# Kernel optimization log

Hardware: AMD Instinct MI355X
Metric: run time of the kernel (lower is better)

Reference implementation:

```python
import jax, jax.numpy as jnp
import numpy as np

# dims: batch, cdd_size, his_size, signal_length, embedding_dim, filter_num, top-k, levels, vocab
B, CDD, HIS, S, E, F, K, L, VOCAB = 32, 5, 50, 20, 300, 150, 30, 3, 50000


def _conv1d(x, w, b, d):
    # x: [N, C_in, S], w: [C_out, C_in, 3], 'same' length via padding=d, dilation=d
    y = jax.lax.conv_general_dilated(x, w, (1,), [(d, d)], rhs_dilation=(d,),
                                     dimension_numbers=('NCW', 'OIW', 'NCW'))
    return y + b[None, :, None]


def _conv3d(x, w, b):
    # x: [N, C_in, D, H, W], padding 1 on all spatial dims
    y = jax.lax.conv_general_dilated(x, w, (1, 1, 1), [(1, 1)] * 3,
                                     dimension_numbers=('NCDHW', 'OIDHW', 'NCDHW'))
    return y + b[None, :, None, None, None]


def _maxpool3(x):
    return jax.lax.reduce_window(x, -jnp.inf, jax.lax.max,
                                 (1, 1, 3, 3, 3), (1, 1, 3, 3, 3), 'VALID')


def setup_inputs() -> dict:
    key = jax.random.key(0)
    ks = jax.random.split(key, 12)
    n = lambda k, s, sc=0.05: jax.random.normal(k, s, dtype=jnp.float32) * sc
    return {
        'candidate_title': jax.random.randint(ks[0], (B, CDD, S), 0, VOCAB),
        'clicked_title': jax.random.randint(ks[1], (B, HIS, S), 0, VOCAB),
        'his_mask': jnp.zeros((B, HIS, 1), dtype=bool),
        'embedding': n(ks[2], (VOCAB, E), 0.1),
        'w1': n(ks[3], (F, E, 3)), 'b1': jnp.zeros((F,), jnp.float32),
        'w2': n(ks[4], (F, F, 3)), 'b2': jnp.zeros((F,), jnp.float32),
        'w3': n(ks[5], (F, F, 3)), 'b3': jnp.zeros((F,), jnp.float32),
        'ln_w': jnp.ones((F,), jnp.float32), 'ln_b': jnp.zeros((F,), jnp.float32),
        'q_words': n(ks[6], (1, F), 1.0), 'q_levels': n(ks[7], (1, F), 1.0),
        'c3d_w1': n(ks[8], (32, L, 3, 3, 3)), 'c3d_b1': jnp.zeros((32,), jnp.float32),
        'c3d_w2': n(ks[9], (16, 32, 3, 3, 3)), 'c3d_b2': jnp.zeros((16,), jnp.float32),
        'ltr_w': n(ks[10], (1, 192)), 'ltr_b': jnp.zeros((1,), jnp.float32),
    }


def reference(candidate_title, clicked_title, his_mask, embedding,
              w1, b1, w2, b2, w3, b3, ln_w, ln_b, q_words, q_levels,
              c3d_w1, c3d_b1, c3d_w2, c3d_b2, ltr_w, ltr_b):
    def ln(x):
        m = x.mean(-1, keepdims=True)
        v = x.var(-1, keepdims=True)  # biased var, matches torch LayerNorm
        return (x - m) / jnp.sqrt(v + 1e-5) * ln_w + ln_b

    scale_e = jnp.sqrt(jnp.float32(E))  # NOTE: original divides by sqrt(embedding_dim)

    def encode(ids):
        nn = ids.shape[1]
        x = embedding[ids].reshape(-1, S, E).transpose(0, 2, 1)  # [N, E, S] (dropout = identity at eval)
        d1 = ln(_conv1d(x, w1, b1, 1).transpose(0, 2, 1))                     # [N, S, F]
        d2 = ln(_conv1d(d1.transpose(0, 2, 1), w2, b2, 2).transpose(0, 2, 1))
        d3 = ln(_conv1d(d2.transpose(0, 2, 1), w3, b3, 3).transpose(0, 2, 1))
        dil = jnp.stack([jax.nn.relu(d1), jax.nn.relu(d2), jax.nn.relu(d3)], axis=2)  # [N, S, L, F]
        dil = dil.reshape(B, nn, S, L, F)
        # level attention with query_levels
        lw = jax.nn.softmax(jnp.einsum('bnslf,f->bnsl', dil, q_levels[0]) / scale_e, axis=-1)
        wf = jnp.einsum('bnsl,bnslf->bnsf', lw, dil)
        # word attention with query_words
        ww = jax.nn.softmax(jnp.einsum('bnsf,f->bns', wf, q_words[0]) / scale_e, axis=-1)
        reprs = jnp.einsum('bns,bnsf->bnf', ww, wf)
        return dil, reprs

    cdd_emb, cdd_repr = encode(candidate_title)   # [B,CDD,S,L,F], [B,CDD,F]
    his_emb, his_repr = encode(clicked_title)     # [B,HIS,S,L,F], [B,HIS,F]

    # news-level attention -> top-k one-hot gating (gather of history news)
    scores = jnp.einsum('bcf,bhf->bch', cdd_repr, his_repr)
    scores = jnp.where(his_mask.transpose(0, 2, 1), -jnp.inf, scores)
    attn = jax.nn.softmax(scores, axis=-1)
    _, idx = jax.lax.top_k(attn, K)                                  # [B,CDD,K]
    his_act = his_emb[jnp.arange(B)[:, None, None], idx]             # [B,CDD,K,S,L,F]

    # fusion tensor: per-level word-word interaction maps
    cdd_t = cdd_emb.transpose(0, 1, 3, 2, 4)       # [B,CDD,L,S,F]
    his_t = his_act.transpose(0, 1, 2, 4, 3, 5)    # [B,CDD,K,L,S,F]
    fusion = jnp.einsum('bclsf,bckltf->bcklst', cdd_t, his_t) / jnp.sqrt(jnp.float32(F))
    fusion = fusion.reshape(B * CDD, K, L, S, S).transpose(0, 2, 1, 3, 4)  # [B*CDD, L, K, S, S]

    h = _maxpool3(jax.nn.relu(_conv3d(fusion, c3d_w1, c3d_b1)))
    h = _maxpool3(jax.nn.relu(_conv3d(h, c3d_w2, c3d_b2)))
    feat = h.reshape(B, CDD, -1)                   # [B, CDD, 192]
    score = jnp.einsum('bcd,d->bc', feat, ltr_w[0]) + ltr_b[0]
    return jax.nn.log_softmax(score, axis=-1)
```

## Files before the change

kernel.cpp:

```cpp
#include <hip/hip_runtime.h>
#include <hip/hip_bf16.h>

#define NB   32
#define NCDD 5
#define NHIS 50
#define SS   20
#define EE   300
#define FF   150
#define KK   30
#define LL   3
#define NSEQ (NB*NCDD + NB*NHIS)
#define NCD  (NB*NCDD)
#define NROW (NSEQ*SS)
#define CONVGRID (NROW/64)

typedef unsigned short u16;
typedef __attribute__((ext_vector_type(8))) short bf16x8;
typedef __attribute__((ext_vector_type(4))) float f32x4;

__device__ __forceinline__ float b2f(u16 v) {
    union { unsigned int u; float f; } c; c.u = ((unsigned int)v) << 16; return c.f;
}
__device__ __forceinline__ u16 f2b(float f) {
    union { float f; unsigned int u; } c; c.f = f;
    unsigned int r = c.u + 0x7FFF + ((c.u >> 16) & 1);
    return (u16)(r >> 16);
}
__device__ __forceinline__ float ldf(const void* p, size_t i, int isbf) {
    return isbf ? b2f(((const u16*)p)[i]) : ((const float*)p)[i];
}
__device__ __forceinline__ float dget(const float* d, size_t i) {
    unsigned int u = ((const unsigned int*)d)[i];
    return b2f((u16)(u & 0xffffu)) + b2f((u16)(u >> 16));
}

__global__ void detect_dtype(const u16* lnw_raw, int* flag) {
    if (threadIdx.x == 0)
        flag[0] = (lnw_raw[0] == 0x3F80 && lnw_raw[1] == 0x3F80) ? 1 : 0;
}

struct CJob { const void* src; float* dst; int n; };
struct CJobs { CJob j[13]; };

__global__ __launch_bounds__(256) void convert_many(CJobs jobs, const int* flagp) {
    int isbf = flagp[0];
    CJob job = jobs.j[blockIdx.x];
    for (int i = threadIdx.x; i < job.n; i += 256) job.dst[i] = ldf(job.src, i, isbf);
}

__global__ __launch_bounds__(256) void repack_wb(const void* w, const int* flagp,
                                                 u16* outh, u16* outl,
                                                 int CIN, int KP, int CV) {
    int isbf = flagp[0];
    int i = blockIdx.x*256 + threadIdx.x;
    if (i >= 160*3*KP) return;
    int g = i % KP; int r = i / KP; int tap = r % 3; int f = r / 3;
    float v = 0.f;
    if (f < FF && g < CV) v = ldf(w, ((size_t)f*CIN + g)*3 + tap, isbf);
    u16 hi = f2b(v);
    u16 lo = f2b(v - b2f(hi));
    size_t o = (size_t)f*(3*KP) + (size_t)tap*KP + g;
    outh[o] = hi; outl[o] = lo;
}

template<int STAGE>
__global__ __launch_bounds__(256, 2) void conv_mfma(const int* __restrict__ flagp,
        const int* __restrict__ cand, const int* __restrict__ clik,
        const void* __restrict__ emb,
        const unsigned int* __restrict__ dprev,
        const u16* __restrict__ wh, const u16* __restrict__ wl,
        const float* __restrict__ bias,
        const float* __restrict__ lnw, const float* __restrict__ lnb,
        unsigned int* __restrict__ dout)
{
    constexpr int KC  = 32;
    constexpr int PAD = 40;
    constexpr int KT  = (STAGE == 0) ? 960 : 480;
    constexpr int NC  = KT / KC;
    constexpr int DIL = (STAGE == 1) ? 2 : 3;
    constexpr int ASZ = 64*PAD, BSZ = 160*PAD;
    constexpr int STG = (2*ASZ + 2*BSZ)*2;
    constexpr int SMB = (STG > 64*164*4) ? STG : 64*164*4;
    __shared__ __align__(16) char smem[SMB];
    u16* Ah = (u16*)smem;
    u16* Al = Ah + ASZ;
    u16* Bh = Al + ASZ;
    u16* Bl = Bh + BSZ;

    const int tid  = threadIdx.x;
    const int row0 = blockIdx.x * 64;
    const int lane = tid & 63, wid = tid >> 6;
    const int wm = wid >> 1, wn = wid & 1;
    const int lr = lane & 15, lk = lane >> 4;
    const int isbf = flagp[0];

    const int arow = tid >> 2, aseg = tid & 3;
    const int grow = row0 + arow;
    const int an   = grow / 20;
    const int as   = grow - an*20;
    int aid[3];
    if constexpr (STAGE == 0) {
        #pragma unroll
        for (int t = 0; t < 3; ++t) {
            int w = as + t - 1;
            aid[t] = ((unsigned)w < 20u) ? ((an < NCD) ? cand[an*SS + w] : clik[(an - NCD)*SS + w])
                                         : -1;
        }
    }

    float xa[8];
    uint4 ra32[2];
    uint4 rb[5];

    auto LOADG = [&](int c) {
        if constexpr (STAGE == 0) {
            int tap = c / 10;
            int e0  = (c - tap*10)*32 + aseg*8;
            int id  = aid[tap];
            float4 x0 = {0.f,0.f,0.f,0.f}, x1 = {0.f,0.f,0.f,0.f};
            if (id >= 0) {
                if (!isbf) {
                    const float* ep = (const float*)emb + (size_t)id*EE + e0;
                    if (e0 < EE)     x0 = *(const float4*)ep;
                    if (e0 + 4 < EE) x1 = *(const float4*)(ep + 4);
                } else {
                    const u16* ep = (const u16*)emb + (size_t)id*EE + e0;
                    float t[8];
                    #pragma unroll
                    for (int j = 0; j < 8; ++j) t[j] = (e0 + j < EE) ? b2f(ep[j]) : 0.f;
                    x0.x=t[0]; x0.y=t[1]; x0.z=t[2]; x0.w=t[3];
                    x1.x=t[4]; x1.y=t[5]; x1.z=t[6]; x1.w=t[7];
                }
            }
            xa[0]=x0.x; xa[1]=x0.y; xa[2]=x0.z; xa[3]=x0.w;
            xa[4]=x1.x; xa[5]=x1.y; xa[6]=x1.z; xa[7]=x1.w;
        } else {
            int tap = c / 5;
            int f0  = (c - tap*5)*32;
            int word = as + DIL*(tap - 1);
            int gbase = f0 + aseg*8;
            ra32[0].x=ra32[0].y=ra32[0].z=ra32[0].w=0u;
            ra32[1].x=ra32[1].y=ra32[1].z=ra32[1].w=0u;
            if ((unsigned)word < 20u && gbase < FF) {
                const unsigned int* p = dprev + (size_t)(an*SS + word)*FF + gbase;
                uint2 q0 = *(const uint2*)(p);
                uint2 q1 = *(const uint2*)(p + 2);
                uint2 q2 = *(const uint2*)(p + 4);
                uint2 q3 = *(const uint2*)(p + 6);
                ra32[0].x = q0.x; ra32[0].y = q0.y; ra32[0].z = q1.x; ra32[0].w = q1.y;
                ra32[1].x = q2.x; ra32[1].y = q2.y; ra32[1].z = q3.x; ra32[1].w = q3.y;
                if (gbase + 7 >= FF) {
                    if (gbase + 1 >= FF) ra32[0].y = 0u;
                    if (gbase + 2 >= FF) ra32[0].z = 0u;
                    if (gbase + 3 >= FF) ra32[0].w = 0u;
                    if (gbase + 4 >= FF) ra32[1].x = 0u;
                    if (gbase + 5 >= FF) ra32[1].y = 0u;
                    if (gbase + 6 >= FF) ra32[1].z = 0u;
                    ra32[1].w = 0u;
                }
            }
        }
        #pragma unroll
        for (int j = 0; j < 5; ++j) {
            int item = tid + j*256;
            const u16* wp = (item < 640) ? wh : wl;
            int rem  = (item < 640) ? item : item - 640;
            rb[j] = *(const uint4*)(wp + (size_t)(rem >> 2)*KT + c*KC + (rem & 3)*8);
        }
    };

    auto WRITE = [&]() {
        uint4 h, l;
        if constexpr (STAGE == 0) {
            u16 hh[8], lo[8];
            #pragma unroll
            for (int j = 0; j < 8; ++j) {
                hh[j] = f2b(xa[j]);
                lo[j] = f2b(xa[j] - b2f(hh[j]));
            }
            h.x = hh[0] | ((unsigned)hh[1] << 16); h.y = hh[2] | ((unsigned)hh[3] << 16);
            h.z = hh[4] | ((unsigned)hh[5] << 16); h.w = hh[6] | ((unsigned)hh[7] << 16);
            l.x = lo[0] | ((unsigned)lo[1] << 16); l.y = lo[2] | ((unsigned)lo[3] << 16);
            l.z = lo[4] | ((unsigned)lo[5] << 16); l.w = lo[6] | ((unsigned)lo[7] << 16);
        } else {
            h.x = (ra32[0].x & 0xffffu) | (ra32[0].y << 16);
            h.y = (ra32[0].z & 0xffffu) | (ra32[0].w << 16);
            h.z = (ra32[1].x & 0xffffu) | (ra32[1].y << 16);
            h.w = (ra32[1].z & 0xffffu) | (ra32[1].w << 16);
            l.x = (ra32[0].x >> 16) | (ra32[0].y & 0xffff0000u);
            l.y = (ra32[0].z >> 16) | (ra32[0].w & 0xffff0000u);
            l.z = (ra32[1].x >> 16) | (ra32[1].y & 0xffff0000u);
            l.w = (ra32[1].z >> 16) | (ra32[1].w & 0xffff0000u);
        }
        *(uint4*)(Ah + arow*PAD + aseg*8) = h;
        *(uint4*)(Al + arow*PAD + aseg*8) = l;
        #pragma unroll
        for (int j = 0; j < 5; ++j) {
            int item = tid + j*256;
            u16* bp = (item < 640) ? Bh : Bl;
            int rem = (item < 640) ? item : item - 640;
            *(uint4*)(bp + (rem >> 2)*PAD + (rem & 3)*8) = rb[j];
        }
    };

    f32x4 acc[2][5];
    #pragma unroll
    for (int mf = 0; mf < 2; ++mf)
        #pragma unroll
        for (int nf = 0; nf < 5; ++nf)
            acc[mf][nf] = (f32x4){0.f,0.f,0.f,0.f};

    auto COMPUTE = [&]() {
        bf16x8 fah[2], fal[2], fbh[5], fbl[5];
        #pragma unroll
        for (int mf = 0; mf < 2; ++mf) {
            fah[mf] = *(const bf16x8*)(Ah + (wm*32 + mf*16 + lr)*PAD + lk*8);
            fal[mf] = *(const bf16x8*)(Al + (wm*32 + mf*16 + lr)*PAD + lk*8);
        }
        #pragma unroll
        for (int nf = 0; nf < 5; ++nf) {
            fbh[nf] = *(const bf16x8*)(Bh + (wn*80 + nf*16 + lr)*PAD + lk*8);
            fbl[nf] = *(const bf16x8*)(Bl + (wn*80 + nf*16 + lr)*PAD + lk*8);
        }
        #pragma unroll
        for (int mf = 0; mf < 2; ++mf)
            #pragma unroll
            for (int nf = 0; nf < 5; ++nf)
                acc[mf][nf] = __builtin_amdgcn_mfma_f32_16x16x32_bf16(fah[mf], fbh[nf], acc[mf][nf], 0, 0, 0);
        #pragma unroll
        for (int mf = 0; mf < 2; ++mf)
            #pragma unroll
            for (int nf = 0; nf < 5; ++nf)
                acc[mf][nf] = __builtin_amdgcn_mfma_f32_16x16x32_bf16(fah[mf], fbl[nf], acc[mf][nf], 0, 0, 0);
        #pragma unroll
        for (int mf = 0; mf < 2; ++mf)
            #pragma unroll
            for (int nf = 0; nf < 5; ++nf)
                acc[mf][nf] = __builtin_amdgcn_mfma_f32_16x16x32_bf16(fal[mf], fbh[nf], acc[mf][nf], 0, 0, 0);
    };

    LOADG(0); WRITE();
    for (int c = 0; c < NC; ++c) {
        if (c + 1 < NC) LOADG(c + 1);
        __syncthreads();
        COMPUTE();
        __syncthreads();
        if (c + 1 < NC) WRITE();
    }

    float* outb = (float*)smem;
    #pragma unroll
    for (int mf = 0; mf < 2; ++mf)
        #pragma unroll
        for (int nf = 0; nf < 5; ++nf)
            #pragma unroll
            for (int r = 0; r < 4; ++r)
                outb[(wm*32 + mf*16 + lk*4 + r)*164 + wn*80 + nf*16 + lr] = acc[mf][nf][r];
    __syncthreads();

    for (int rl = wid*16; rl < wid*16 + 16; ++rl) {
        float vv[3]; float sum = 0.f, sq = 0.f;
        #pragma unroll
        for (int j = 0; j < 3; ++j) {
            int f = lane + j*64;
            float v = 0.f;
            if (f < FF) v = outb[rl*164 + f] + bias[f];
            vv[j] = v; sum += v; sq += v*v;
        }
        #pragma unroll
        for (int off = 32; off; off >>= 1) { sum += __shfl_down(sum, off); sq += __shfl_down(sq, off); }
        sum = __shfl(sum, 0); sq = __shfl(sq, 0);
        float m = sum / FF, var = sq / FF - m*m, inv = rsqrtf(var + 1e-5f);
        #pragma unroll
        for (int j = 0; j < 3; ++j) {
            int f = lane + j*64;
            if (f < FF) {
                float v = (vv[j] - m) * inv * lnw[f] + lnb[f];
                u16 hi = f2b(v);
                unsigned int lo = (unsigned int)f2b(v - b2f(hi));
                dout[(size_t)(row0 + rl)*FF + f] = (unsigned int)hi | (lo << 16);
            }
        }
    }
}

__global__ __launch_bounds__(256) void lvwd_attn(const float* d1, const float* d2, const float* d3,
                                                 const float* ql, const float* qw, float* reprs) {
    __shared__ float wfs[SS*FF];
    __shared__ float scs[SS];
    int n = blockIdx.x, tid = threadIdx.x;
    int wave = tid >> 6, lane = tid & 63;
    for (int s = wave; s < SS; s += 4) {
        size_t base = ((size_t)n*SS + s) * FF;
        float v[3][3];
        float dt[3] = {0.f, 0.f, 0.f};
        #pragma unroll
        for (int j = 0; j < 3; ++j) {
            int f = lane + j*64;
            float q = (f < FF) ? ql[f] : 0.f;
            float x0 = (f < FF) ? fmaxf(dget(d1, base+f), 0.f) : 0.f;
            float x1 = (f < FF) ? fmaxf(dget(d2, base+f), 0.f) : 0.f;
            float x2 = (f < FF) ? fmaxf(dget(d3, base+f), 0.f) : 0.f;
            v[0][j] = x0; v[1][j] = x1; v[2][j] = x2;
            dt[0] += x0*q; dt[1] += x1*q; dt[2] += x2*q;
        }
        #pragma unroll
        for (int off = 32; off; off >>= 1) {
            dt[0] += __shfl_xor(dt[0], off);
            dt[1] += __shfl_xor(dt[1], off);
            dt[2] += __shfl_xor(dt[2], off);
        }
        const float sc = 0.057735026918962584f;
        float a0 = dt[0]*sc, a1 = dt[1]*sc, a2 = dt[2]*sc;
        float mx = fmaxf(a0, fmaxf(a1, a2));
        float e0 = expf(a0-mx), e1 = expf(a1-mx), e2 = expf(a2-mx);
        float den = e0+e1+e2;
        float l0 = e0/den, l1 = e1/den, l2 = e2/den;
        #pragma unroll
        for (int j = 0; j < 3; ++j) {
            int f = lane + j*64;
            if (f < FF) wfs[s*FF + f] = l0*v[0][j] + l1*v[1][j] + l2*v[2][j];
        }
    }
    __syncthreads();
    if (wave == 0) {
        if (lane < SS) {
            float a = 0.f;
            for (int f = 0; f < FF; ++f) a += wfs[lane*FF + f]*qw[f];
            scs[lane] = a * 0.057735026918962584f;
        }
        float mx = -1e30f;
        #pragma unroll
        for (int s = 0; s < SS; ++s) mx = fmaxf(mx, scs[s]);
        float ww[SS]; float den = 0.f;
        #pragma unroll
        for (int s = 0; s < SS; ++s) { ww[s] = expf(scs[s]-mx); den += ww[s]; }
        float inv = 1.f/den;
        for (int f = lane; f < FF; f += 64) {
            float a = 0.f;
            #pragma unroll
            for (int s = 0; s < SS; ++s) a += ww[s]*wfs[s*FF + f];
            reprs[(size_t)n*FF + f] = a*inv;
        }
    }
}

__global__ __launch_bounds__(256) void score_kernel(const float* reprs, const unsigned char* mask,
                                                    float* scores) {
    int i = blockIdx.x*256 + threadIdx.x;
    if (i >= NB*NCDD*NHIS) return;
    int b = i/(NCDD*NHIS); int r = i%(NCDD*NHIS); int h = r%NHIS; int c = r/NHIS;
    const float* cr = reprs + (size_t)(b*NCDD + c)*FF;
    const float* hr = reprs + (size_t)(NCD + b*NHIS + h)*FF;
    float a = 0.f;
    for (int f = 0; f < FF; ++f) a += cr[f]*hr[f];
    if (mask[b*NHIS + h]) a = -1e30f;
    scores[i] = a;
}

__global__ __launch_bounds__(64) void topk_kernel(const float* scores, int* idx) {
    int i = blockIdx.x*64 + threadIdx.x;
    if (i >= NB*NCDD) return;
    float sc[NHIS];
    const float* sp = scores + i*NHIS;
    for (int h = 0; h < NHIS; ++h) sc[h] = sp[h];
    for (int k = 0; k < KK; ++k) {
        int best = 0; float bv = -1e38f;
        for (int h = 0; h < NHIS; ++h) { if (sc[h] > bv) { bv = sc[h]; best = h; } }
        idx[i*KK + k] = best;
        sc[best] = -1e38f;
    }
}

__global__ __launch_bounds__(256) void fusion_kernel(const float* d1, const float* d2, const float* d3,
                                                     const int* idx, float* fus) {
    constexpr int RS  = 168;
    constexpr int TSZ = 32*RS;
    __shared__ __align__(16) u16 smem[4*TSZ];
    u16* Ah = smem;
    u16* Al = smem + TSZ;
    u16* Hh = smem + 2*TSZ;
    u16* Hl = smem + 3*TSZ;
    int blk = blockIdx.x;
    int k = blk % KK; int r2 = blk / KK; int l = r2 % LL; int bc = r2 / LL;
    int b = bc / NCDD;
    int nh = NCD + b*NHIS + idx[bc*KK + k];
    const float* dl = (l == 0) ? d1 : ((l == 1) ? d2 : d3);
    const unsigned int* Ap = (const unsigned int*)dl + (size_t)bc*SS*FF;
    const unsigned int* Hp = (const unsigned int*)dl + (size_t)nh*SS*FF;
    int tid = threadIdx.x;
    for (int i = tid; i < 4*TSZ/8; i += 256)
        *(uint4*)(smem + (size_t)i*8) = (uint4){0u,0u,0u,0u};
    __syncthreads();
    for (int item = tid; item < 760; item += 256) {
        int side = item >= 380;
        int rem  = side ? item - 380 : item;
        int row  = rem / 19, f0 = (rem - row*19)*8;
        const unsigned int* p = (side ? Hp : Ap) + row*FF + f0;
        unsigned int q[8];
        #pragma unroll
        for (int j = 0; j < 8; j += 2) {
            uint2 t2 = {0u, 0u};
            if (f0 + j < FF) t2 = *(const uint2*)(p + j);
            q[j] = t2.x; q[j+1] = t2.y;
        }
        unsigned int hh[8], ll[8];
        #pragma unroll
        for (int j = 0; j < 8; ++j) {
            unsigned int u = q[j];
            float f = b2f((u16)(u & 0xffffu)) + b2f((u16)(u >> 16));
            int keep = (f > 0.f);
            hh[j] = keep ? (u & 0xffffu) : 0u;
            ll[j] = keep ? (u >> 16)     : 0u;
        }
        uint4 h, lo;
        h.x  = hh[0] | (hh[1] << 16); h.y  = hh[2] | (hh[3] << 16);
        h.z  = hh[4] | (hh[5] << 16); h.w  = hh[6] | (hh[7] << 16);
        lo.x = ll[0] | (ll[1] << 16); lo.y = ll[2] | (ll[3] << 16);
        lo.z = ll[4] | (ll[5] << 16); lo.w = ll[6] | (ll[7] << 16);
        u16* dh = (side ? Hh : Ah) + row*RS + f0;
        u16* dL = (side ? Hl : Al) + row*RS + f0;
        *(uint4*)dh = h;
        *(uint4*)dL = lo;
    }
    __syncthreads();
    const int lane = tid & 63, wid = tid >> 6;
    const int wm = wid >> 1, wn = wid & 1;
    const int lr = lane & 15, lk = lane >> 4;
    f32x4 acc = {0.f, 0.f, 0.f, 0.f};
    #pragma unroll
    for (int c = 0; c < 5; ++c) {
        bf16x8 fah = *(const bf16x8*)(Ah + (wm*16 + lr)*RS + c*32 + lk*8);
        bf16x8 fal = *(const bf16x8*)(Al + (wm*16 + lr)*RS + c*32 + lk*8);
        bf16x8 fbh = *(const bf16x8*)(Hh + (wn*16 + lr)*RS + c*32 + lk*8);
        bf16x8 fbl = *(const bf16x8*)(Hl + (wn*16 + lr)*RS + c*32 + lk*8);
        acc = __builtin_amdgcn_mfma_f32_16x16x32_bf16(fah, fbh, acc, 0, 0, 0);
        acc = __builtin_amdgcn_mfma_f32_16x16x32_bf16(fah, fbl, acc, 0, 0, 0);
        acc = __builtin_amdgcn_mfma_f32_16x16x32_bf16(fal, fbh, acc, 0, 0, 0);
    }
    #pragma unroll
    for (int r = 0; r < 4; ++r) {
        int s = wm*16 + lk*4 + r, t = wn*16 + lr;
        if (s < SS && t < SS)
            fus[(size_t)blk*400 + s*20 + t] = acc[r] * 0.08164965809277261f;
    }
}

__global__ __launch_bounds__(256) void c3d1_kernel(const float* __restrict__ fus,
                                                   const float* __restrict__ w,
                                                   const float* __restrict__ bias,
                                                   float* __restrict__ h1) {
    __shared__ float Sin[3*5*22*22];
    __shared__ float Wls[32*81];
    int blk = blockIdx.x;
    int dz = blk % 10; int bc = blk / 10;
    int tid = threadIdx.x;
    for (int i = tid; i < 32*81; i += 256) Wls[i] = w[i];
    int z0 = dz*3 - 1;
    for (int i = tid; i < 3*5*22*22; i += 256) {
        int x = i % 22; int r = i / 22;
        int y = r % 22; r /= 22;
        int zl = r % 5; int ic = r / 5;
        int zz = z0 + zl, yy = y - 1, xx = x - 1;
        float v = 0.f;
        if ((unsigned)zz < 30u && (unsigned)yy < 20u && (unsigned)xx < 20u)
            v = fus[((size_t)(bc*3 + ic)*30 + zz)*400 + yy*20 + xx];
        Sin[i] = v;
    }
    __syncthreads();
    for (int item = tid; item < 1152; item += 256) {
        int oc = item & 31; int dydx = item >> 5;
        int dy = dydx / 6, dx = dydx % 6;
        float acc[27];
        #pragma unroll
        for (int j = 0; j < 27; ++j) acc[j] = 0.f;
        int ybase = dy*3, xbase = dx*3;
        for (int ic = 0; ic < 3; ++ic) {
            #pragma unroll
            for (int zl = 0; zl < 5; ++zl) {
                float p[5][5];
                const float* sp = &Sin[((ic*5 + zl)*22 + ybase)*22 + xbase];
                #pragma unroll
                for (int yy = 0; yy < 5; ++yy)
                    #pragma unroll
                    for (int xx = 0; xx < 5; ++xx) p[yy][xx] = sp[yy*22 + xx];
                #pragma unroll
                for (int pz = 0; pz < 3; ++pz) {
                    int kz = zl - pz;
                    if (kz < 0 || kz > 2) continue;
                    const float* wv = &Wls[oc*81 + ic*27 + kz*9];
                    #pragma unroll
                    for (int ky = 0; ky < 3; ++ky)
                    #pragma unroll
                    for (int kx = 0; kx < 3; ++kx) {
                        float wgt = wv[ky*3 + kx];
                        #pragma unroll
                        for (int py = 0; py < 3; ++py)
                        #pragma unroll
                        for (int px = 0; px < 3; ++px)
                            acc[pz*9 + py*3 + px] += p[py+ky][px+kx] * wgt;
                    }
                }
            }
        }
        float best = -1e30f;
        #pragma unroll
        for (int j = 0; j < 27; ++j) best = fmaxf(best, acc[j]);
        h1[((size_t)(bc*32 + oc)*10 + dz)*36 + dydx] = fmaxf(best + bias[oc], 0.f);
    }
}

#define W2STR 865
__global__ __launch_bounds__(192) void c3d2_kernel(const float* __restrict__ h1,
                                                   const float* __restrict__ w,
                                                   const float* __restrict__ bias,
                                                   float* __restrict__ h2) {
    __shared__ float Sin[32*360];
    __shared__ float Wls[4*W2STR];
    int blk = blockIdx.x;
    int og = blk & 3; int bc = blk >> 2;
    int ocbase = og*4;
    int tid = threadIdx.x;
    for (int i = tid; i < 32*360; i += 192) Sin[i] = h1[(size_t)bc*32*360 + i];
    for (int i = tid; i < 4*864; i += 192) {
        int ol = i / 864, rem = i - ol*864;
        Wls[ol*W2STR + rem] = w[(size_t)(ocbase + ol)*864 + rem];
    }
    __syncthreads();
    if (tid < 144) {
        int ol = tid & 3; int yx = tid >> 2;
        int y = yx / 6, x = yx % 6;
        float acc[10];
        #pragma unroll
        for (int z = 0; z < 10; ++z) acc[z] = 0.f;
        for (int ic = 0; ic < 32; ++ic) {
            #pragma unroll
            for (int ky = 0; ky < 3; ++ky) {
                int yy = y + ky - 1;
                if ((unsigned)yy >= 6u) continue;
                #pragma unroll
                for (int kx = 0; kx < 3; ++kx) {
                    int xx = x + kx - 1;
                    if ((unsigned)xx >= 6u) continue;
                    float col[12];
                    col[0] = 0.f; col[11] = 0.f;
                    #pragma unroll
                    for (int zz = 0; zz < 10; ++zz)
                        col[zz+1] = Sin[(ic*10 + zz)*36 + yy*6 + xx];
                    #pragma unroll
                    for (int kz = 0; kz < 3; ++kz) {
                        float wgt = Wls[ol*W2STR + ic*27 + kz*9 + ky*3 + kx];
                        #pragma unroll
                        for (int z = 0; z < 10; ++z)
                            acc[z] += col[z + kz] * wgt;
                    }
                }
            }
        }
        int oc = ocbase + ol;
        float b = bias[oc];
        #pragma unroll
        for (int z = 0; z < 10; ++z)
            h2[(size_t)(bc*16 + oc)*360 + z*36 + yx] = fmaxf(acc[z] + b, 0.f);
    }
}

__global__ __launch_bounds__(256) void pool2_kernel(const float* h2, float* h2p) {
    int i = blockIdx.x*256 + threadIdx.x;
    if (i >= NCD*16*3*2*2) return;
    int dx = i % 2; int r = i/2;
    int dy = r % 2; r /= 2;
    int dz = r % 3; r /= 3;
    int oc = r % 16; r /= 16;
    int bc = r;
    const float* hp = h2 + ((size_t)bc*16 + oc)*360;
    float best = -1e30f;
    for (int pz = 0; pz < 3; ++pz)
    for (int py = 0; py < 3; ++py)
    for (int px = 0; px < 3; ++px) {
        int z = dz*3+pz, y = dy*3+py, x = dx*3+px;
        best = fmaxf(best, hp[(z*6 + y)*6 + x]);
    }
    h2p[i] = best;
}

__global__ __launch_bounds__(64) void ltr_kernel(const float* h2p, const float* lw,
                                                 const float* lb, float* sc) {
    int i = blockIdx.x*64 + threadIdx.x;
    if (i >= NB*NCDD) return;
    const float* f = h2p + (size_t)i*192;
    float a = lb[0];
    for (int d = 0; d < 192; ++d) a += f[d]*lw[d];
    sc[i] = a;
}

__global__ __launch_bounds__(64) void lsm_kernel(const float* sc, const int* flagp, void* out) {
    int b = threadIdx.x;
    if (b >= NB) return;
    int isbf = flagp[0];
    float v[NCDD]; float mx = -1e30f;
    #pragma unroll
    for (int c = 0; c < NCDD; ++c) { v[c] = sc[b*NCDD + c]; mx = fmaxf(mx, v[c]); }
    float den = 0.f;
    #pragma unroll
    for (int c = 0; c < NCDD; ++c) den += expf(v[c]-mx);
    float lse = mx + logf(den);
    #pragma unroll
    for (int c = 0; c < NCDD; ++c) {
        float o = v[c] - lse;
        if (isbf) ((u16*)out)[b*NCDD + c] = f2b(o);
        else      ((float*)out)[b*NCDD + c] = o;
    }
}

extern "C" void kernel_launch(void* const* d_in, const int* in_sizes, int n_in,
                              void* d_out, int out_size, void* d_ws, size_t ws_size,
                              hipStream_t stream) {
    const int* cand  = (const int*)d_in[0];
    const int* clik  = (const int*)d_in[1];
    const unsigned char* mask = (const unsigned char*)d_in[2];
    const void* emb  = d_in[3];
    const void* w1   = d_in[4];
    const void* b1   = d_in[5];
    const void* w2   = d_in[6];
    const void* b2   = d_in[7];
    const void* w3   = d_in[8];
    const void* b3   = d_in[9];
    const void* lnw  = d_in[10];
    const void* lnb  = d_in[11];
    const void* qw   = d_in[12];
    const void* ql   = d_in[13];
    const void* cw1  = d_in[14];
    const void* cb1  = d_in[15];
    const void* cw2  = d_in[16];
    const void* cb2  = d_in[17];
    const void* lw   = d_in[18];
    const void* lb   = d_in[19];

    char* wsb = (char*)d_ws;
    size_t off = 0;
    auto A = [&](size_t bytes) -> void* {
        void* p = wsb + off;
        off = (off + bytes + 255) & ~(size_t)255;
        return p;
    };
    int*   flag = (int*)A(4);
    float* b1f  = (float*)A(FF*4);
    float* b2f  = (float*)A(FF*4);
    float* b3f  = (float*)A(FF*4);
    float* lnwf = (float*)A(FF*4);
    float* lnbf = (float*)A(FF*4);
    float* qwf  = (float*)A(FF*4);
    float* qlf  = (float*)A(FF*4);
    float* c1w  = (float*)A(32*3*27*4);
    float* c1b  = (float*)A(32*4);
    float* c2w  = (float*)A(16*32*27*4);
    float* c2b  = (float*)A(16*4);
    float* lwf  = (float*)A(192*4);
    float* lbf  = (float*)A(4);
    u16*   wt1h = (u16*)A((size_t)160*960*2);
    u16*   wt1l = (u16*)A((size_t)160*960*2);
    u16*   wt2h = (u16*)A((size_t)160*480*2);
    u16*   wt2l = (u16*)A((size_t)160*480*2);
    u16*   wt3h = (u16*)A((size_t)160*480*2);
    u16*   wt3l = (u16*)A((size_t)160*480*2);
    float* d1   = (float*)A((size_t)NSEQ*SS*FF*4);
    float* d2   = (float*)A((size_t)NSEQ*SS*FF*4);
    float* d3   = (float*)A((size_t)NSEQ*SS*FF*4);
    float* fus  = (float*)A((size_t)NCD*LL*KK*SS*SS*4);
    float* reprs= (float*)A((size_t)NSEQ*FF*4);
    float* scb  = (float*)A((size_t)NB*NCDD*NHIS*4);
    int*   idx  = (int*)A((size_t)NB*NCDD*KK*4);
    float* h1   = d1;
    float* h2   = d2;
    float* h2p  = d3;
    float* fsc  = (float*)((char*)d3 + 256*1024);
    (void)ws_size; (void)in_sizes; (void)n_in; (void)out_size;

    detect_dtype<<<1, 64, 0, stream>>>((const u16*)lnw, flag);

    CJobs jobs;
    jobs.j[0]  = {b1,  b1f,  FF};
    jobs.j[1]  = {b2,  b2f,  FF};
    jobs.j[2]  = {b3,  b3f,  FF};
    jobs.j[3]  = {lnw, lnwf, FF};
    jobs.j[4]  = {lnb, lnbf, FF};
    jobs.j[5]  = {qw,  qwf,  FF};
    jobs.j[6]  = {ql,  qlf,  FF};
    jobs.j[7]  = {cw1, c1w,  32*3*27};
    jobs.j[8]  = {cb1, c1b,  32};
    jobs.j[9]  = {cw2, c2w,  16*32*27};
    jobs.j[10] = {cb2, c2b,  16};
    jobs.j[11] = {lw,  lwf,  192};
    jobs.j[12] = {lb,  lbf,  1};
    convert_many<<<13, 256, 0, stream>>>(jobs, flag);
    repack_wb<<<(160*960 + 255)/256, 256, 0, stream>>>(w1, flag, wt1h, wt1l, EE, 320, 300);
    repack_wb<<<(160*480 + 255)/256, 256, 0, stream>>>(w2, flag, wt2h, wt2l, FF, 160, 150);
    repack_wb<<<(160*480 + 255)/256, 256, 0, stream>>>(w3, flag, wt3h, wt3l, FF, 160, 150);

    conv_mfma<0><<<CONVGRID, 256, 0, stream>>>(flag, cand, clik, emb, nullptr,
                                               wt1h, wt1l, b1f, lnwf, lnbf, (unsigned int*)d1);
    conv_mfma<1><<<CONVGRID, 256, 0, stream>>>(flag, cand, clik, emb, (const unsigned int*)d1,
                                               wt2h, wt2l, b2f, lnwf, lnbf, (unsigned int*)d2);
    conv_mfma<2><<<CONVGRID, 256, 0, stream>>>(flag, cand, clik, emb, (const unsigned int*)d2,
                                               wt3h, wt3l, b3f, lnwf, lnbf, (unsigned int*)d3);

    lvwd_attn<<<NSEQ, 256, 0, stream>>>(d1, d2, d3, qlf, qwf, reprs);
    score_kernel<<<(NB*NCDD*NHIS + 255)/256, 256, 0, stream>>>(reprs, mask, scb);
    topk_kernel<<<(NB*NCDD + 63)/64, 64, 0, stream>>>(scb, idx);
    fusion_kernel<<<NCD*LL*KK, 256, 0, stream>>>(d1, d2, d3, idx, fus);
    c3d1_kernel<<<NCD*10, 256, 0, stream>>>(fus, c1w, c1b, h1);
    c3d2_kernel<<<NCD*4, 192, 0, stream>>>(h1, c2w, c2b, h2);
    pool2_kernel<<<(NCD*16*3*2*2 + 255)/256, 256, 0, stream>>>(h2, h2p);
    ltr_kernel<<<(NB*NCDD + 63)/64, 64, 0, stream>>>(h2p, lwf, lbf, fsc);
    lsm_kernel<<<1, 64, 0, stream>>>(fsc, flag, d_out);
}
```

Measured before the change: 862.4 us.

## Rewrite second 3D conv as MFMA implicit GEMM with split-bf16 operands

The second Conv3d (32 to 16 channels) moves from a scalar FP32 per-thread loop to an implicit-GEMM MFMA kernel. The first conv now writes its output as packed hi/lo bf16 pairs in a channel-last layout, and a new repack kernel splits the conv weights into hi/lo bf16 in tap-major order. The new kernel stages zero-padded z-planes in LDS and issues three bf16 MFMAs per tile to approximate FP32 accuracy. This trades scalar FMA throughput for matrix cores, but uses one block per sample instead of four, which lowers parallelism.

```diff
diff --git a/kernel.cpp b/kernel.cpp
--- a/kernel.cpp
+++ b/kernel.cpp
@@ -17,6 +17,7 @@
 typedef unsigned short u16;
 typedef __attribute__((ext_vector_type(8))) short bf16x8;
 typedef __attribute__((ext_vector_type(4))) float f32x4;
+typedef __attribute__((ext_vector_type(4))) unsigned int u32x4;
 
 __device__ __forceinline__ float b2f(u16 v) {
     union { unsigned int u; float f; } c; c.u = ((unsigned int)v) << 16; return c.f;
@@ -32,6 +33,12 @@
 __device__ __forceinline__ float dget(const float* d, size_t i) {
     unsigned int u = ((const unsigned int*)d)[i];
     return b2f((u16)(u & 0xffffu)) + b2f((u16)(u >> 16));
+}
+__device__ __forceinline__ bf16x8 ld_frag8(const u16* p) {
+    uint2 q0 = *(const uint2*)(p);
+    uint2 q1 = *(const uint2*)(p + 4);
+    u32x4 t; t.x = q0.x; t.y = q0.y; t.z = q1.x; t.w = q1.y;
+    return __builtin_bit_cast(bf16x8, t);
 }
 
 __global__ void detect_dtype(const u16* lnw_raw, int* flag) {
@@ -60,6 +67,18 @@
     u16 hi = f2b(v);
     u16 lo = f2b(v - b2f(hi));
     size_t o = (size_t)f*(3*KP) + (size_t)tap*KP + g;
+    outh[o] = hi; outl[o] = lo;
+}
+
+__global__ __launch_bounds__(256) void repack_w2(const void* w, const int* flagp,
+                                                 u16* outh, u16* outl) {
+    int isbf = flagp[0];
+    int i = blockIdx.x*256 + threadIdx.x;
+    if (i >= 16*864) return;
+    int ic = i & 31; int r = i >> 5; int tap = r % 27; int oc = r / 27;
+    float v = ldf(w, ((size_t)oc*32 + ic)*27 + tap, isbf);
+    u16 hi = f2b(v); u16 lo = f2b(v - b2f(hi));
+    size_t o = (size_t)oc*864 + tap*32 + ic;
     outh[o] = hi; outl[o] = lo;
 }
 
@@ -449,7 +468,7 @@
 __global__ __launch_bounds__(256) void c3d1_kernel(const float* __restrict__ fus,
                                                    const float* __restrict__ w,
                                                    const float* __restrict__ bias,
-                                                   float* __restrict__ h1) {
+                                                   unsigned int* __restrict__ h1p) {
     __shared__ float Sin[3*5*22*22];
     __shared__ float Wls[32*81];
     int blk = blockIdx.x;
@@ -506,62 +525,75 @@
         float best = -1e30f;
         #pragma unroll
         for (int j = 0; j < 27; ++j) best = fmaxf(best, acc[j]);
-        h1[((size_t)(bc*32 + oc)*10 + dz)*36 + dydx] = fmaxf(best + bias[oc], 0.f);
-    }
-}
-
-#define W2STR 865
-__global__ __launch_bounds__(192) void c3d2_kernel(const float* __restrict__ h1,
-                                                   const float* __restrict__ w,
+        float v = fmaxf(best + bias[oc], 0.f);
+        u16 hi = f2b(v);
+        unsigned int lo = (unsigned int)f2b(v - b2f(hi));
+        h1p[((size_t)(bc*10 + dz)*36 + dydx)*32 + oc] = (unsigned int)hi | (lo << 16);
+    }
+}
+
+#define ARS 36
+#define APL (36*ARS)
+__global__ __launch_bounds__(256) void c3d2_kernel(const unsigned int* __restrict__ h1p,
+                                                   const u16* __restrict__ wh,
+                                                   const u16* __restrict__ wl,
                                                    const float* __restrict__ bias,
                                                    float* __restrict__ h2) {
-    __shared__ float Sin[32*360];
-    __shared__ float Wls[4*W2STR];
-    int blk = blockIdx.x;
-    int og = blk & 3; int bc = blk >> 2;
-    int ocbase = og*4;
-    int tid = threadIdx.x;
-    for (int i = tid; i < 32*360; i += 192) Sin[i] = h1[(size_t)bc*32*360 + i];
-    for (int i = tid; i < 4*864; i += 192) {
-        int ol = i / 864, rem = i - ol*864;
-        Wls[ol*W2STR + rem] = w[(size_t)(ocbase + ol)*864 + rem];
+    __shared__ __align__(16) u16 Ah[12*APL];
+    __shared__ __align__(16) u16 Al[12*APL];
+    int bc = blockIdx.x, tid = threadIdx.x;
+    for (int i = tid; i < 2*APL; i += 256) {
+        int a = (i < APL) ? i : (11*APL + i - APL);
+        Ah[a] = 0; Al[a] = 0;
+    }
+    for (int i = tid; i < 10*36*32; i += 256) {
+        int ic = i & 31; int r = i >> 5; int yx = r % 36; int z = r / 36;
+        unsigned int u = h1p[(size_t)bc*11520 + i];
+        int a = (z + 1)*APL + yx*ARS + ic;
+        Ah[a] = (u16)(u & 0xffffu);
+        Al[a] = (u16)(u >> 16);
     }
     __syncthreads();
-    if (tid < 144) {
-        int ol = tid & 3; int yx = tid >> 2;
-        int y = yx / 6, x = yx % 6;
-        float acc[10];
-        #pragma unroll
-        for (int z = 0; z < 10; ++z) acc[z] = 0.f;
-        for (int ic = 0; ic < 32; ++ic) {
-            #pragma unroll
-            for (int ky = 0; ky < 3; ++ky) {
-                int yy = y + ky - 1;
-                if ((unsigned)yy >= 6u) continue;
-                #pragma unroll
-                for (int kx = 0; kx < 3; ++kx) {
-                    int xx = x + kx - 1;
-                    if ((unsigned)xx >= 6u) continue;
-                    float col[12];
-                    col[0] = 0.f; col[11] = 0.f;
-                    #pragma unroll
-                    for (int zz = 0; zz < 10; ++zz)
-                        col[zz+1] = Sin[(ic*10 + zz)*36 + yy*6 + xx];
-                    #pragma unroll
-                    for (int kz = 0; kz < 3; ++kz) {
-                        float wgt = Wls[ol*W2STR + ic*27 + kz*9 + ky*3 + kx];
-                        #pragma unroll
-                        for (int z = 0; z < 10; ++z)
-                            acc[z] += col[z + kz] * wgt;
-                    }
-                }
-            }
-        }
-        int oc = ocbase + ol;
-        float b = bias[oc];
-        #pragma unroll
-        for (int z = 0; z < 10; ++z)
-            h2[(size_t)(bc*16 + oc)*360 + z*36 + yx] = fmaxf(acc[z] + b, 0.f);
+    const int lane = tid & 63, wid = tid >> 6;
+    const int lr = lane & 15, lk = lane >> 4;
+    const int t0 = wid*6;
+    int rr[6], rz[6], ry[6], rx[6];
+    #pragma unroll
+    for (int ti = 0; ti < 6; ++ti) {
+        int r = (t0 + ti)*16 + lr;
+        rr[ti] = r;
+        int z = r / 36; int yx = r - z*36; int y = yx / 6;
+        rz[ti] = z; ry[ti] = y; rx[ti] = yx - y*6;
+    }
+    f32x4 acc[6];
+    #pragma unroll
+    for (int ti = 0; ti < 6; ++ti) acc[ti] = (f32x4){0.f,0.f,0.f,0.f};
+    for (int tap = 0; tap < 27; ++tap) {
+        int kz = tap/9, kyx = tap - kz*9, ky = kyx/3, kx = kyx - ky*3;
+        bf16x8 fbh = *(const bf16x8*)(wh + (size_t)lr*864 + tap*32 + lk*8);
+        bf16x8 fbl = *(const bf16x8*)(wl + (size_t)lr*864 + tap*32 + lk*8);
+        #pragma unroll
+        for (int ti = 0; ti < 6; ++ti) {
+            int yy = ry[ti] + ky - 1;
+            int xx = rx[ti] + kx - 1;
+            bool ok = (rr[ti] < 360) && ((unsigned)yy < 6u) && ((unsigned)xx < 6u);
+            int a = ok ? ((rz[ti] + kz)*APL + (yy*6 + xx)*ARS + lk*8) : (lk*8);
+            bf16x8 fah = ld_frag8(Ah + a);
+            bf16x8 fal = ld_frag8(Al + a);
+            acc[ti] = __builtin_amdgcn_mfma_f32_16x16x32_bf16(fah, fbh, acc[ti], 0, 0, 0);
+            acc[ti] = __builtin_amdgcn_mfma_f32_16x16x32_bf16(fah, fbl, acc[ti], 0, 0, 0);
+            acc[ti] = __builtin_amdgcn_mfma_f32_16x16x32_bf16(fal, fbh, acc[ti], 0, 0, 0);
+        }
+    }
+    float b = bias[lr];
+    #pragma unroll
+    for (int ti = 0; ti < 6; ++ti) {
+        #pragma unroll
+        for (int r4 = 0; r4 < 4; ++r4) {
+            int row = (t0 + ti)*16 + lk*4 + r4;
+            if (row < 360)
+                h2[((size_t)bc*16 + lr)*360 + row] = fmaxf(acc[ti][r4] + b, 0.f);
+        }
     }
 }
 
@@ -664,6 +696,8 @@
     u16*   wt2l = (u16*)A((size_t)160*480*2);
     u16*   wt3h = (u16*)A((size_t)160*480*2);
     u16*   wt3l = (u16*)A((size_t)160*480*2);
+    u16*   w2ch = (u16*)A((size_t)16*864*2);
+    u16*   w2cl = (u16*)A((size_t)16*864*2);
     float* d1   = (float*)A((size_t)NSEQ*SS*FF*4);
     float* d2   = (float*)A((size_t)NSEQ*SS*FF*4);
     float* d3   = (float*)A((size_t)NSEQ*SS*FF*4);
@@ -671,7 +705,7 @@
     float* reprs= (float*)A((size_t)NSEQ*FF*4);
     float* scb  = (float*)A((size_t)NB*NCDD*NHIS*4);
     int*   idx  = (int*)A((size_t)NB*NCDD*KK*4);
-    float* h1   = d1;
+    unsigned int* h1p = (unsigned int*)d1;
     float* h2   = d2;
     float* h2p  = d3;
     float* fsc  = (float*)((char*)d3 + 256*1024);
@@ -697,6 +731,7 @@
     repack_wb<<<(160*960 + 255)/256, 256, 0, stream>>>(w1, flag, wt1h, wt1l, EE, 320, 300);
     repack_wb<<<(160*480 + 255)/256, 256, 0, stream>>>(w2, flag, wt2h, wt2l, FF, 160, 150);
     repack_wb<<<(160*480 + 255)/256, 256, 0, stream>>>(w3, flag, wt3h, wt3l, FF, 160, 150);
+    repack_w2<<<(16*864 + 255)/256, 256, 0, stream>>>(cw2, flag, w2ch, w2cl);
 
     conv_mfma<0><<<CONVGRID, 256, 0, stream>>>(flag, cand, clik, emb, nullptr,
                                                wt1h, wt1l, b1f, lnwf, lnbf, (unsigned int*)d1);
@@ -709,8 +744,8 @@
     score_kernel<<<(NB*NCDD*NHIS + 255)/256, 256, 0, stream>>>(reprs, mask, scb);
     topk_kernel<<<(NB*NCDD + 63)/64, 64, 0, stream>>>(scb, idx);
     fusion_kernel<<<NCD*LL*KK, 256, 0, stream>>>(d1, d2, d3, idx, fus);
-    c3d1_kernel<<<NCD*10, 256, 0, stream>>>(fus, c1w, c1b, h1);
-    c3d2_kernel<<<NCD*4, 192, 0, stream>>>(h1, c2w, c2b, h2);
+    c3d1_kernel<<<NCD*10, 256, 0, stream>>>(fus, c1w, c1b, h1p);
+    c3d2_kernel<<<NCD, 256, 0, stream>>>(h1p, w2ch, w2cl, c2b, h2);
     pool2_kernel<<<(NCD*16*3*2*2 + 255)/256, 256, 0, stream>>>(h2, h2p);
     ltr_kernel<<<(NB*NCDD + 63)/64, 64, 0, stream>>>(h2p, lwf, lbf, fsc);
     lsm_kernel<<<1, 64, 0, stream>>>(fsc, flag, d_out);
```

After: 815.5 us. 1.06x faster.
